# Performance work log

Measured on AMD Instinct MI355X. Metric: run time of the kernel, lower is better.

## Reference

```python
import jax, jax.numpy as jnp
import numpy as np

U = 1024  # utterance_size
H = 1024  # hidden_size
B = 32
T = 256


def _gru_cell(x, h, w_ih, w_hh, b_ih, b_hh):
    # torch.nn.GRUCell math
    gi = x @ w_ih.T + b_ih
    gh = h @ w_hh.T + b_hh
    i_r, i_z, i_n = jnp.split(gi, 3, axis=-1)
    h_r, h_z, h_n = jnp.split(gh, 3, axis=-1)
    r = jax.nn.sigmoid(i_r + h_r)
    z = jax.nn.sigmoid(i_z + h_z)
    n = jnp.tanh(i_n + r * h_n)
    return (1.0 - z) * n + z * h


def setup_inputs() -> dict:
    key = jax.random.key(0)
    ks = jax.random.split(key, 15)
    su = 1.0 / np.sqrt(U)
    sh = 1.0 / np.sqrt(H)

    def unif(k, shape, s):
        return jax.random.uniform(k, shape, jnp.float32, -s, s)

    inputs = jax.random.normal(ks[0], (B, T, U), jnp.float32)
    global_W = jax.random.normal(ks[1], (U, U), jnp.float32)
    gW_ih = unif(ks[2], (3 * U, U), su)
    gW_hh = unif(ks[3], (3 * U, U), su)
    gb_ih = unif(ks[4], (3 * U,), su)
    gb_hh = unif(ks[5], (3 * U,), su)
    pW_ih = unif(ks[6], (3 * U, U), su)
    pW_hh = unif(ks[7], (3 * U, U), su)
    pb_ih = unif(ks[8], (3 * U,), su)
    pb_hh = unif(ks[9], (3 * U,), su)
    eW_ih = unif(ks[10], (3 * H, U), sh)
    eW_hh = unif(ks[11], (3 * H, H), sh)
    eb_ih = unif(ks[12], (3 * H,), sh)
    eb_hh = unif(ks[13], (3 * H,), sh)
    return dict(inputs=inputs, global_W=global_W,
                gW_ih=gW_ih, gW_hh=gW_hh, gb_ih=gb_ih, gb_hh=gb_hh,
                pW_ih=pW_ih, pW_hh=pW_hh, pb_ih=pb_ih, pb_hh=pb_hh,
                eW_ih=eW_ih, eW_hh=eW_hh, eb_ih=eb_ih, eb_hh=eb_hh)


def _forward(inputs, global_W, gW_ih, gW_hh, gb_ih, gb_hh,
             pW_ih, pW_hh, pb_ih, pb_hh, eW_ih, eW_hh, eb_ih, eb_hh):
    Bb, Tt, Uu = inputs.shape
    Hh = eW_hh.shape[-1]
    x = jnp.transpose(inputs, (1, 0, 2))  # (T, B, U)
    hist0 = jnp.zeros((Tt + 1, Bb, Uu), inputs.dtype)  # global_s history, index 0 = zero init
    g0 = jnp.zeros((Bb, Uu), inputs.dtype)
    p0_0 = jnp.zeros((Bb, Uu), inputs.dtype)
    p1_0 = jnp.zeros((Bb, Uu), inputs.dtype)
    e0 = jnp.zeros((Bb, Hh), inputs.dtype)
    time_idx = jnp.arange(Tt + 1)

    def step(carry, xi):
        hist, g, p0, p1, e = carry
        ut, i = xi
        is_even = (i % 2) == 0
        p_cur = jnp.where(is_even, p0, p1)  # party_s[cur_party]
        g_new = _gru_cell(ut + p_cur, g, gW_ih, gW_hh, gb_ih, gb_hh)
        hist = hist.at[i + 1].set(g_new)  # appended but NOT attended this step
        # attention over global_s[0:i+1] (zero init + g_0..g_{i-1})
        q = ut @ global_W  # (B, U)
        scores = jnp.einsum('tbu,bu->tb', hist, q)  # (T+1, B)
        mask = time_idx[:, None] <= i
        scores = jnp.where(mask, scores, -jnp.inf)
        alpha = jax.nn.softmax(scores, axis=0)  # softmax over history dim
        ct = jnp.einsum('tb,tbu->bu', alpha, hist)
        p_new = _gru_cell(ut + ct, p_cur, pW_ih, pW_hh, pb_ih, pb_hh)
        p0 = jnp.where(is_even, p_new, p0)
        p1 = jnp.where(is_even, p1, p_new)
        e_new = _gru_cell(p_new, e, eW_ih, eW_hh, eb_ih, eb_hh)
        return (hist, g_new, p0, p1, e_new), e_new

    _, outs = jax.lax.scan(step, (hist0, g0, p0_0, p1_0, e0), (x, jnp.arange(Tt)))
    return jnp.transpose(outs, (1, 0, 2))  # (B, T, H)


def reference(inputs, global_W, gW_ih, gW_hh, gb_ih, gb_hh,
              pW_ih, pW_hh, pb_ih, pb_hh, eW_ih, eW_hh, eb_ih, eb_hh):
    return _forward(inputs, global_W, gW_ih, gW_hh, gb_ih, gb_hh,
                    pW_ih, pW_hh, pb_ih, pb_hh, eW_ih, eW_hh, eb_ih, eb_hh)
```

## Files before the change

### kernel.cpp

```cpp
#include <hip/hip_runtime.h>
#include <math.h>

#define UU 1024
#define BB 32
#define TT 256
#define NCHUNK 2
#define GRIDN 256
#define RING 32

#define WPS   6291456u
#define WCELL (2u * WPS)
#define SR  0u
#define SZ  2097152u
#define SNX 4194304u
#define SNH 5242880u
#define APS   65536u
#define ASLOT (2u * APS)
#define AEX(u, b) ((((((u) >> 5) * 4 + (((u) >> 3) & 3)) * 32 + (b)) * 8) + ((u) & 7))

#define SCR_OFF  131072
#define RED_OFF  147456
#define FLAG_OFF 147520
#define LDSB     147584

typedef __attribute__((ext_vector_type(8))) short bf16x8;
typedef __attribute__((ext_vector_type(4))) float f32x4;
#define MF(a, b, c) __builtin_amdgcn_mfma_f32_16x16x32_bf16((a), (b), (c), 0, 0, 0)

__device__ __forceinline__ ushort bf16rne(float v) {
    uint x = __float_as_uint(v);
    uint r = (x + 0x7fffu + ((x >> 16) & 1u)) >> 16;
    return (ushort)r;
}
__device__ __forceinline__ float ubf2f(ushort u) {
    return __uint_as_float(((uint)u) << 16);
}
__device__ __forceinline__ void split2(float v, ushort& h, ushort& l) {
    h = bf16rne(v);
    l = bf16rne(v - ubf2f(h));
}
__device__ __forceinline__ void store_f32_sc(float* p, float v) {
    asm volatile("global_store_dword %0, %1, off sc1" :: "v"(p), "v"(v) : "memory");
}
__device__ __forceinline__ void store_u16_sc(ushort* p, ushort v) {
    uint vv = v;
    asm volatile("global_store_short %0, %1, off sc1" :: "v"(p), "v"(vv) : "memory");
}
__device__ __forceinline__ void vm_drain() {
    asm volatile("s_waitcnt vmcnt(0)" ::: "memory");
}
__device__ __forceinline__ float load_f32_ag(const float* p) {
    return __hip_atomic_load(p, __ATOMIC_RELAXED, __HIP_MEMORY_SCOPE_AGENT);
}
__device__ __forceinline__ int load_i32_ag(const int* p) {
    return __hip_atomic_load(p, __ATOMIC_RELAXED, __HIP_MEMORY_SCOPE_AGENT);
}
__device__ __forceinline__ bf16x8 load_frag_ag(const ushort* p) {
    union { unsigned long long q[2]; bf16x8 v; } u;
    u.q[0] = __hip_atomic_load((const unsigned long long*)p,
                               __ATOMIC_RELAXED, __HIP_MEMORY_SCOPE_AGENT);
    u.q[1] = __hip_atomic_load((const unsigned long long*)(p + 4),
                               __ATOMIC_RELAXED, __HIP_MEMORY_SCOPE_AGENT);
    return u.v;
}

__global__ void packw_kernel(const float* __restrict__ gWih, const float* __restrict__ gWhh,
                             const float* __restrict__ pWih, const float* __restrict__ pWhh,
                             const float* __restrict__ eWih, const float* __restrict__ eWhh,
                             ushort* __restrict__ wpack) {
    int cellb = blockIdx.x / 12288;
    int tile = blockIdx.x - cellb * 12288;
    const float* Wih = (cellb == 0) ? gWih : (cellb == 1) ? pWih : eWih;
    const float* Whh = (cellb == 0) ? gWhh : (cellb == 1) ? pWhh : eWhh;
    ushort* wp = wpack + (size_t)cellb * WCELL;
    int sec, jt, ks, nks;
    size_t soff;
    if (tile < 8192) {
        sec = tile >> 12; int l = tile & 4095; jt = l >> 6; ks = l & 63; nks = 64;
        soff = sec ? SZ : SR;
    } else {
        int l2 = tile - 8192; sec = 2 + (l2 >> 11); int l = l2 & 2047; jt = l >> 5; ks = l & 31; nks = 32;
        soff = (sec == 2) ? SNX : SNH;
    }
    int p = threadIdx.x;
    int e0 = (p & 3) * 2, ul = (p >> 2) & 15, hi = p >> 6;
    int u = jt * 16 + ul;
    int kk = ks * 32 + hi * 8 + e0;
    float2 w;
    if (sec < 2) {
        int row = (sec ? 1024 : 0) + u;
        if (kk < 1024) w = *(const float2*)&Wih[(size_t)row * UU + kk];
        else           w = *(const float2*)&Whh[(size_t)row * UU + kk - 1024];
    } else if (sec == 2) {
        w = *(const float2*)&Wih[(size_t)(2048 + u) * UU + kk];
    } else {
        w = *(const float2*)&Whh[(size_t)(2048 + u) * UU + kk];
    }
    ushort h0, l0, h1, l1;
    split2(w.x, h0, l0); split2(w.y, h1, l1);
    size_t ob = soff + ((((size_t)jt * nks + ks) * 4 + hi) * 16 + ul) * 8 + e0;
    *(uint*)(wp + ob)       = (uint)h0 | ((uint)h1 << 16);
    *(uint*)(wp + WPS + ob) = (uint)l0 | ((uint)l1 << 16);
}

__global__ __launch_bounds__(256)
void qall_kernel(const float* __restrict__ x,
                 const float* __restrict__ gW,
                 float* __restrict__ q) {
    __shared__ float xs[16][257];
    __shared__ float gws[16][128];
    const int r0 = blockIdx.x * 256, n0 = blockIdx.y * 128;
    const int tid = threadIdx.x;
    const int tr = tid & 31, tn = tid >> 5;
    float acc[8][16];
    #pragma unroll
    for (int i = 0; i < 8; ++i)
        #pragma unroll
        for (int j = 0; j < 16; ++j) acc[i][j] = 0.f;
    for (int k0 = 0; k0 < UU; k0 += 16) {
        {
            int rr = tid >> 2;
            const int f4 = (tid & 3) * 4;
            #pragma unroll
            for (int it = 0; it < 4; ++it, rr += 64) {
                const int r = r0 + rr;
                const int tt = r >> 5, bb = r & 31;
                float4 v = *(const float4*)&x[((size_t)bb * TT + tt) * UU + k0 + f4];
                xs[f4][rr] = v.x; xs[f4 + 1][rr] = v.y;
                xs[f4 + 2][rr] = v.z; xs[f4 + 3][rr] = v.w;
            }
        }
        {
            int kr = tid >> 5;
            const int nn = (tid & 31) * 4;
            #pragma unroll
            for (int it = 0; it < 2; ++it, kr += 8) {
                float4 v = *(const float4*)&gW[(size_t)(k0 + kr) * UU + n0 + nn];
                *(float4*)&gws[kr][nn] = v;
            }
        }
        __syncthreads();
        #pragma unroll
        for (int kk = 0; kk < 16; ++kk) {
            float xv[8];
            #pragma unroll
            for (int i = 0; i < 8; ++i) xv[i] = xs[kk][tr + 32 * i];
            float gv[16];
            #pragma unroll
            for (int j4 = 0; j4 < 4; ++j4) {
                float4 g = *(const float4*)&gws[kk][tn * 16 + j4 * 4];
                gv[j4 * 4] = g.x; gv[j4 * 4 + 1] = g.y;
                gv[j4 * 4 + 2] = g.z; gv[j4 * 4 + 3] = g.w;
            }
            #pragma unroll
            for (int i = 0; i < 8; ++i)
                #pragma unroll
                for (int j = 0; j < 16; ++j)
                    acc[i][j] += xv[i] * gv[j];
        }
        __syncthreads();
    }
    #pragma unroll
    for (int i = 0; i < 8; ++i) {
        const int r = r0 + tr + 32 * i;
        #pragma unroll
        for (int j4 = 0; j4 < 4; ++j4) {
            float4 v = {acc[i][j4 * 4], acc[i][j4 * 4 + 1],
                        acc[i][j4 * 4 + 2], acc[i][j4 * 4 + 3]};
            *(float4*)&q[(size_t)r * UU + n0 + tn * 16 + j4 * 4] = v;
        }
    }
}

__global__ void init_kernel(const float* __restrict__ inputs,
                            const float* __restrict__ gbih, const float* __restrict__ gbhh,
                            const float* __restrict__ pbih, const float* __restrict__ pbhh,
                            const float* __restrict__ ebih, const float* __restrict__ ebhh,
                            float* __restrict__ hist, float* __restrict__ Pf,
                            ushort* __restrict__ gpack, ushort* __restrict__ ppack,
                            ushort* __restrict__ epack, float* __restrict__ biasp,
                            int* __restrict__ cnt, int* __restrict__ bar) {
    if (blockIdx.x == 0) {
        if (threadIdx.x < 32) cnt[threadIdx.x] = 0;
        for (int i = threadIdx.x; i < 1024; i += 256) bar[i] = 0;
    }
    if (blockIdx.x < 128) {
        int i = blockIdx.x * 256 + threadIdx.x;
        int b = i >> 10, u = i & 1023;
        hist[i] = 0.f;
        Pf[i] = 0.f; Pf[32768 + i] = 0.f;
        int ex = AEX(u, b);
        int eh = ex + 32768;
        gpack[eh] = 0; gpack[APS + eh] = 0;
        ppack[eh] = 0; ppack[APS + eh] = 0;
        ppack[ASLOT + eh] = 0; ppack[ASLOT + APS + eh] = 0;
        epack[eh] = 0; epack[APS + eh] = 0;
        float x0 = inputs[((size_t)b * TT + 0) * UU + u];
        float x1 = inputs[((size_t)b * TT + 1) * UU + u];
        ushort h, l;
        split2(x0, h, l); gpack[ex] = h; gpack[APS + ex] = l;
        split2(x1, h, l); gpack[ASLOT + ex] = h; gpack[ASLOT + APS + ex] = l;
    } else {
        int idx = (blockIdx.x - 128) * 256 + threadIdx.x;
        int cell = idx >> 12, g4 = (idx >> 10) & 3, u = idx & 1023;
        const float* bih = (cell == 0) ? gbih : (cell == 1) ? pbih : ebih;
        const float* bhh = (cell == 0) ? gbhh : (cell == 1) ? pbhh : ebhh;
        float v;
        if (g4 == 0) v = bih[u] + bhh[u];
        else if (g4 == 1) v = bih[1024 + u] + bhh[1024 + u];
        else if (g4 == 2) v = bih[2048 + u];
        else v = bhh[2048 + u];
        biasp[idx] = v;
    }
}

__global__ __launch_bounds__(512)
__attribute__((amdgpu_waves_per_eu(2)))
void persist_kernel(const float* __restrict__ inputs,
                    const ushort* __restrict__ wpack,
                    const float* __restrict__ biasp,
                    ushort* __restrict__ gpack, ushort* __restrict__ ppack,
                    ushort* __restrict__ epack,
                    float* __restrict__ hist, float* __restrict__ Pf,
                    const float* __restrict__ qall,
                    float* __restrict__ out,
                    float* __restrict__ attC, float* __restrict__ attML,
                    int* __restrict__ cnt, int* __restrict__ bar) {
    extern __shared__ char smraw[];
    float* lds_scr  = (float*)(smraw + SCR_OFF);
    float* lds_red  = (float*)(smraw + RED_OFF);
    int*   lds_flag = (int*)(smraw + FLAG_OFF);

    const int blk = blockIdx.x, tid = threadIdx.x;
    const int cell = blk >> 6, jt = blk & 63;
    const int w = tid >> 6, lane = tid & 63;
    const int l15 = lane & 15, hi4 = lane >> 4;
    const int ab = blk & 31, ac = (blk >> 5) & 1;
    const ushort* wp = wpack + (size_t)cell * WCELL;

    if (cell < 3) {
        bf16x8 whiR[8], whiZ[8], whiN[8], wloN[8];
        const int ebt = tid >> 8, eli = (tid >> 2) & 63, ei = tid & 3;
        const int eb = ebt * 16 + (eli & 15);
        const int eu = jt * 16 + (eli >> 4) * 4 + ei;
        const int eex = AEX(eu, eb);
        #pragma unroll
        for (int i = 0; i < 8; ++i) {
            const int ks = w * 8 + i;
            const size_t aoff = ((size_t)(jt * 256 + ks * 4 + hi4)) * 128 + (size_t)l15 * 8;
            whiR[i] = *(const bf16x8*)(wp + SR + aoff);
            whiZ[i] = *(const bf16x8*)(wp + SZ + aoff);
            bf16x8 rlo = *(const bf16x8*)(wp + SR + WPS + aoff);
            bf16x8 zlo = *(const bf16x8*)(wp + SZ + WPS + aoff);
            *(bf16x8*)(smraw + (((w * 16 + i) * 64 + lane) << 4)) = rlo;
            *(bf16x8*)(smraw + (((w * 16 + 8 + i) * 64 + lane) << 4)) = zlo;
            const int ksn = (w & 3) * 8 + i;
            const size_t noff = ((size_t)(jt * 128 + ksn * 4 + hi4)) * 128 + (size_t)l15 * 8;
            const size_t sN = (w < 4) ? SNX : SNH;
            whiN[i] = *(const bf16x8*)(wp + sN + noff);
            wloN[i] = *(const bf16x8*)(wp + sN + WPS + noff);
        }
        const float* bc = biasp + cell * 4096;
        const float bR = bc[eu], bZ = bc[1024 + eu];
        const float bNI = bc[2048 + eu], bNH = bc[3072 + eu];
        ushort* apk = (cell == 0) ? gpack : (cell == 1) ? ppack : epack;
        __syncthreads();

        for (int tc = 0; tc < TT; ++tc) {
            if (w == 0) {
                const int* wptr; int wneed;
                if (cell == 0) {
                    if (lane == 0)      { wptr = bar;       wneed = tc; }
                    else if (lane == 1) { wptr = bar + 32;  wneed = tc - 1; }
                    else                { wptr = bar;       wneed = -2147483647; }
                } else if (cell == 1) {
                    if (lane < 32)       { wptr = bar + 512 + lane * 16; wneed = tc + 1; }
                    else if (lane == 32) { wptr = bar + 32; wneed = tc - 1; }
                    else if (lane == 33) { wptr = bar + 64; wneed = tc - 31; }
                    else                 { wptr = bar;      wneed = -2147483647; }
                } else {
                    if (lane == 0)      { wptr = bar + 32;  wneed = tc + 1; }
                    else if (lane == 1) { wptr = bar + 64;  wneed = tc; }
                    else                { wptr = bar;       wneed = -2147483647; }
                }
                while (!__all(load_i32_ag(wptr) >= wneed))
                    __builtin_amdgcn_s_sleep(8);
            }
            __syncthreads();
            f32x4 aR0 = {0,0,0,0}, aR1 = {0,0,0,0};
            f32x4 aZ0 = {0,0,0,0}, aZ1 = {0,0,0,0};
            f32x4 aN0 = {0,0,0,0}, aN1 = {0,0,0,0};
            const ushort* ap = apk + (size_t)(tc & (RING - 1)) * ASLOT;
            const ushort* bbp = ap + ((size_t)hi4 * 32 + l15) * 8;
            #pragma unroll
            for (int i = 0; i < 8; ++i) {
                const int ks = w * 8 + i;
                const ushort* bp = bbp + (size_t)ks * 1024;
                bf16x8 bh0 = load_frag_ag(bp);
                bf16x8 bh1 = load_frag_ag(bp + 128);
                bf16x8 bl0 = load_frag_ag(bp + APS);
                bf16x8 bl1 = load_frag_ag(bp + APS + 128);
                bf16x8 rlo = *(const bf16x8*)(smraw + (((w * 16 + i) * 64 + lane) << 4));
                bf16x8 zlo = *(const bf16x8*)(smraw + (((w * 16 + 8 + i) * 64 + lane) << 4));
                aR0 = MF(whiR[i], bh0, aR0); aR0 = MF(whiR[i], bl0, aR0); aR0 = MF(rlo, bh0, aR0);
                aR1 = MF(whiR[i], bh1, aR1); aR1 = MF(whiR[i], bl1, aR1); aR1 = MF(rlo, bh1, aR1);
                aZ0 = MF(whiZ[i], bh0, aZ0); aZ0 = MF(whiZ[i], bl0, aZ0); aZ0 = MF(zlo, bh0, aZ0);
                aZ1 = MF(whiZ[i], bh1, aZ1); aZ1 = MF(whiZ[i], bl1, aZ1); aZ1 = MF(zlo, bh1, aZ1);
                aN0 = MF(whiN[i], bh0, aN0); aN0 = MF(whiN[i], bl0, aN0); aN0 = MF(wloN[i], bh0, aN0);
                aN1 = MF(whiN[i], bh1, aN1); aN1 = MF(whiN[i], bl1, aN1); aN1 = MF(wloN[i], bh1, aN1);
            }
            float R, Z, iN, hN;
            *(f32x4*)&lds_scr[((0 * 8 + w) * 64 + lane) * 4] = aR0;
            *(f32x4*)&lds_scr[((1 * 8 + w) * 64 + lane) * 4] = aR1;
            __syncthreads();
            {
                float s = 0.f;
                #pragma unroll
                for (int w2 = 0; w2 < 8; ++w2) s += lds_scr[((ebt * 8 + w2) * 64 + eli) * 4 + ei];
                R = s;
            }
            __syncthreads();
            *(f32x4*)&lds_scr[((0 * 8 + w) * 64 + lane) * 4] = aZ0;
            *(f32x4*)&lds_scr[((1 * 8 + w) * 64 + lane) * 4] = aZ1;
            __syncthreads();
            {
                float s = 0.f;
                #pragma unroll
                for (int w2 = 0; w2 < 8; ++w2) s += lds_scr[((ebt * 8 + w2) * 64 + eli) * 4 + ei];
                Z = s;
            }
            __syncthreads();
            *(f32x4*)&lds_scr[((0 * 8 + w) * 64 + lane) * 4] = aN0;
            *(f32x4*)&lds_scr[((1 * 8 + w) * 64 + lane) * 4] = aN1;
            __syncthreads();
            {
                float si = 0.f, sh = 0.f;
                #pragma unroll
                for (int w2 = 0; w2 < 4; ++w2) si += lds_scr[((ebt * 8 + w2) * 64 + eli) * 4 + ei];
                #pragma unroll
                for (int w2 = 4; w2 < 8; ++w2) sh += lds_scr[((ebt * 8 + w2) * 64 + eli) * 4 + ei];
                iN = si; hN = sh;
            }
            {
                float hprev;
                if (cell == 0)      hprev = hist[((size_t)tc * BB + eb) * UU + eu];
                else if (cell == 1) hprev = load_f32_ag(&Pf[(size_t)(tc & (RING - 1)) * BB * UU + (size_t)eb * UU + eu]);
                else                hprev = (tc > 0) ? out[((size_t)eb * TT + tc - 1) * UU + eu] : 0.f;
                const float r = 1.f / (1.f + expf(-(R + bR)));
                const float z = 1.f / (1.f + expf(-(Z + bZ)));
                const float n2 = tanhf(iN + bNI + r * (hN + bNH));
                const float val = (1.f - z) * n2 + z * hprev;
                ushort vh, vl; split2(val, vh, vl);
                if (cell == 0) {
                    store_f32_sc(&hist[((size_t)(tc + 1) * BB + eb) * UU + eu], val);
                    ushort* d = gpack + (size_t)((tc + 1) & (RING - 1)) * ASLOT;
                    store_u16_sc(d + eex + 32768, vh);
                    store_u16_sc(d + APS + eex + 32768, vl);
                } else if (cell == 1) {
                    ushort* d = epack + (size_t)(tc & (RING - 1)) * ASLOT;
                    store_u16_sc(d + eex, vh);
                    store_u16_sc(d + APS + eex, vl);
                    if (tc + 2 < TT) {
                        store_f32_sc(&Pf[(size_t)((tc + 2) & (RING - 1)) * BB * UU + (size_t)eb * UU + eu], val);
                        ushort* d2 = ppack + (size_t)((tc + 2) & (RING - 1)) * ASLOT;
                        store_u16_sc(d2 + eex + 32768, vh);
                        store_u16_sc(d2 + APS + eex + 32768, vl);
                        const float gx = val + inputs[((size_t)eb * TT + tc + 2) * UU + eu];
                        ushort gh, gl; split2(gx, gh, gl);
                        ushort* d3 = gpack + (size_t)((tc + 2) & (RING - 1)) * ASLOT;
                        store_u16_sc(d3 + eex, gh);
                        store_u16_sc(d3 + APS + eex, gl);
                    }
                } else {
                    store_f32_sc(&out[((size_t)eb * TT + tc) * UU + eu], val);
                    if (tc + 1 < TT) {
                        ushort* d = epack + (size_t)((tc + 1) & (RING - 1)) * ASLOT;
                        store_u16_sc(d + eex + 32768, vh);
                        store_u16_sc(d + APS + eex + 32768, vl);
                    }
                }
            }
            vm_drain();
            __syncthreads();
            if (tid == 0) {
                int* ring = bar + 128 + cell * 128 + (tc & 3) * 32;
                int old = __hip_atomic_fetch_add(ring, 1, __ATOMIC_RELAXED,
                                                 __HIP_MEMORY_SCOPE_AGENT);
                if ((old & 63) == 63) {
                    (void)__hip_atomic_fetch_max(bar + cell * 32, tc + 1,
                                                 __ATOMIC_RELAXED, __HIP_MEMORY_SCOPE_AGENT);
                }
            }
        }
    } else {
        int* fin = bar + 512 + ab * 16;
        for (int t = 0; t < TT; ++t) {
            if (w == 0) {
                const int* wptr; int wneed;
                if (lane == 0)      { wptr = bar; wneed = t; }
                else if (lane == 1) { wptr = fin; wneed = t; }
                else                { wptr = bar; wneed = -2147483647; }
                while (!__all(load_i32_ag(wptr) >= wneed))
                    __builtin_amdgcn_s_sleep(8);
            }
            __syncthreads();
            const int slot = t & 3;
            float* aC = attC + (((size_t)slot * NCHUNK + ac) * BB + ab) * UU;
            float* aML = attML + (((size_t)slot * NCHUNK + ac) * BB + ab) * 2;
            const int nt2 = t + 1;
            const int cstr = (nt2 + NCHUNK - 1) / NCHUNK;
            const int r0 = ac * cstr;
            const int r1x = r0 + cstr;
            const int r1 = (r1x < nt2) ? r1x : nt2;
            const int n = r1 - r0;
            if (n <= 0) {
                #pragma unroll
                for (int rep = 0; rep < 2; ++rep)
                    store_f32_sc(aC + tid + rep * 512, 0.f);
                if (tid == 0) {
                    store_f32_sc(aML, -INFINITY);
                    store_f32_sc(aML + 1, 0.f);
                }
            } else {
                const float* qb = qall + ((size_t)t * BB + ab) * UU;
                float4 q0 = *(const float4*)&qb[lane * 4];
                float4 q1 = *(const float4*)&qb[256 + lane * 4];
                float4 q2 = *(const float4*)&qb[512 + lane * 4];
                float4 q3 = *(const float4*)&qb[768 + lane * 4];
                float m_run = -INFINITY, l_run = 0.f;
                float4 c0 = {0,0,0,0}, c1 = {0,0,0,0}, c2 = {0,0,0,0}, c3 = {0,0,0,0};
                for (int tp = r0 + w; tp < r1; tp += 8) {
                    const float* hr = hist + ((size_t)tp * BB + ab) * UU;
                    float4 h0 = *(const float4*)&hr[lane * 4];
                    float4 h1 = *(const float4*)&hr[256 + lane * 4];
                    float4 h2 = *(const float4*)&hr[512 + lane * 4];
                    float4 h3 = *(const float4*)&hr[768 + lane * 4];
                    float s = h0.x*q0.x + h0.y*q0.y + h0.z*q0.z + h0.w*q0.w
                            + h1.x*q1.x + h1.y*q1.y + h1.z*q1.z + h1.w*q1.w
                            + h2.x*q2.x + h2.y*q2.y + h2.z*q2.z + h2.w*q2.w
                            + h3.x*q3.x + h3.y*q3.y + h3.z*q3.z + h3.w*q3.w;
                    #pragma unroll
                    for (int off = 32; off; off >>= 1) s += __shfl_xor(s, off);
                    const float mn = fmaxf(m_run, s);
                    const float sc = expf(m_run - mn);
                    const float e2 = expf(s - mn);
                    c0.x = c0.x*sc + e2*h0.x; c0.y = c0.y*sc + e2*h0.y; c0.z = c0.z*sc + e2*h0.z; c0.w = c0.w*sc + e2*h0.w;
                    c1.x = c1.x*sc + e2*h1.x; c1.y = c1.y*sc + e2*h1.y; c1.z = c1.z*sc + e2*h1.z; c1.w = c1.w*sc + e2*h1.w;
                    c2.x = c2.x*sc + e2*h2.x; c2.y = c2.y*sc + e2*h2.y; c2.z = c2.z*sc + e2*h2.z; c2.w = c2.w*sc + e2*h2.w;
                    c3.x = c3.x*sc + e2*h3.x; c3.y = c3.y*sc + e2*h3.y; c3.z = c3.z*sc + e2*h3.z; c3.w = c3.w*sc + e2*h3.w;
                    l_run = l_run * sc + e2;
                    m_run = mn;
                }
                *(float4*)&lds_scr[w * 512 + lane * 4] = c0;
                *(float4*)&lds_scr[w * 512 + 256 + lane * 4] = c1;
                if (lane == 0) { lds_red[w] = m_run; lds_red[8 + w] = l_run; }
                __syncthreads();
                float M = lds_red[0];
                #pragma unroll
                for (int k = 1; k < 8; ++k) M = fmaxf(M, lds_red[k]);
                float ww[8], L = 0.f;
                #pragma unroll
                for (int k = 0; k < 8; ++k) { ww[k] = expf(lds_red[k] - M); L += ww[k] * lds_red[8 + k]; }
                if (tid == 0) {
                    store_f32_sc(aML, M);
                    store_f32_sc(aML + 1, L);
                }
                {
                    float s = 0.f;
                    #pragma unroll
                    for (int w2 = 0; w2 < 8; ++w2) s += ww[w2] * lds_scr[w2 * 512 + tid];
                    store_f32_sc(aC + tid, s);
                }
                __syncthreads();
                *(float4*)&lds_scr[w * 512 + lane * 4] = c2;
                *(float4*)&lds_scr[w * 512 + 256 + lane * 4] = c3;
                __syncthreads();
                {
                    float s = 0.f;
                    #pragma unroll
                    for (int w2 = 0; w2 < 8; ++w2) s += ww[w2] * lds_scr[w2 * 512 + tid];
                    store_f32_sc(aC + 512 + tid, s);
                }
            }
            vm_drain();
            __syncthreads();
            if (tid == 0) {
                int old = __hip_atomic_fetch_add(cnt + ab, 1, __ATOMIC_RELAXED,
                                                 __HIP_MEMORY_SCOPE_AGENT);
                lds_flag[0] = (old & 1);
            }
            __syncthreads();
            if (lds_flag[0]) {
                float mm[NCHUNK], ll[NCHUNK];
                #pragma unroll
                for (int c = 0; c < NCHUNK; ++c) {
                    const float* ml = attML + (((size_t)slot * NCHUNK + c) * BB + ab) * 2;
                    mm[c] = load_f32_ag(ml);
                    ll[c] = load_f32_ag(ml + 1);
                }
                float M2 = mm[0];
                #pragma unroll
                for (int c = 1; c < NCHUNK; ++c) M2 = fmaxf(M2, mm[c]);
                float den = 0.f, wc[NCHUNK];
                #pragma unroll
                for (int c = 0; c < NCHUNK; ++c) { wc[c] = expf(mm[c] - M2); den += wc[c] * ll[c]; }
                const float inv = 1.f / den;
                ushort* d = ppack + (size_t)(t & (RING - 1)) * ASLOT;
                #pragma unroll
                for (int rep = 0; rep < 2; ++rep) {
                    const int e = tid + rep * 512;
                    float s3 = 0.f;
                    #pragma unroll
                    for (int c = 0; c < NCHUNK; ++c)
                        s3 += wc[c] * load_f32_ag(&attC[(((size_t)slot * NCHUNK + c) * BB + ab) * UU + e]);
                    const float xv = s3 * inv + inputs[((size_t)ab * TT + t) * UU + e];
                    ushort vh2, vl2; split2(xv, vh2, vl2);
                    const int ex2 = AEX(e, ab);
                    store_u16_sc(d + ex2, vh2);
                    store_u16_sc(d + APS + ex2, vl2);
                }
                vm_drain();
            }
            __syncthreads();
            if (tid == 0 && lds_flag[0])
                __hip_atomic_fetch_add(fin, 1, __ATOMIC_RELAXED, __HIP_MEMORY_SCOPE_AGENT);
        }
    }
}

extern "C" void kernel_launch(void* const* d_in, const int* in_sizes, int n_in,
                              void* d_out, int out_size, void* d_ws, size_t ws_size,
                              hipStream_t stream) {
    (void)in_sizes; (void)n_in; (void)out_size; (void)ws_size;
    const float* inputs = (const float*)d_in[0];
    const float* gW   = (const float*)d_in[1];
    const float* gWih = (const float*)d_in[2];
    const float* gWhh = (const float*)d_in[3];
    const float* gbih = (const float*)d_in[4];
    const float* gbhh = (const float*)d_in[5];
    const float* pWih = (const float*)d_in[6];
    const float* pWhh = (const float*)d_in[7];
    const float* pbih = (const float*)d_in[8];
    const float* pbhh = (const float*)d_in[9];
    const float* eWih = (const float*)d_in[10];
    const float* eWhh = (const float*)d_in[11];
    const float* ebih = (const float*)d_in[12];
    const float* ebhh = (const float*)d_in[13];
    float* out = (float*)d_out;

    char* ws = (char*)d_ws;
    size_t off = 0;
    auto alloc = [&](size_t bytes) {
        void* p = ws + off;
        off += (bytes + 255) & ~(size_t)255;
        return p;
    };
    ushort* wpack = (ushort*)alloc((size_t)3 * WCELL * 2);
    ushort* gpack = (ushort*)alloc((size_t)RING * ASLOT * 2);
    ushort* ppack = (ushort*)alloc((size_t)RING * ASLOT * 2);
    ushort* epack = (ushort*)alloc((size_t)RING * ASLOT * 2);
    float* hist  = (float*)alloc((size_t)(TT + 1) * BB * UU * 4);
    float* qall  = (float*)alloc((size_t)TT * BB * UU * 4);
    float* Pf    = (float*)alloc((size_t)RING * BB * UU * 4);
    float* biasp = (float*)alloc((size_t)3 * 4096 * 4);
    float* attC  = (float*)alloc((size_t)4 * NCHUNK * BB * UU * 4);
    float* attML = (float*)alloc((size_t)4 * NCHUNK * BB * 2 * 4);
    int*   cnt   = (int*)alloc(32 * 4);
    int*   bar   = (int*)alloc(1024 * 4);

    packw_kernel<<<36864, 256, 0, stream>>>(gWih, gWhh, pWih, pWhh, eWih, eWhh, wpack);
    qall_kernel<<<dim3(32, 8), 256, 0, stream>>>(inputs, gW, qall);
    init_kernel<<<176, 256, 0, stream>>>(inputs, gbih, gbhh, pbih, pbhh, ebih, ebhh,
                                         hist, Pf, gpack, ppack, epack, biasp, cnt, bar);

    hipFuncSetAttribute((const void*)persist_kernel,
                        hipFuncAttributeMaxDynamicSharedMemorySize, LDSB);
    void* args[] = {(void*)&inputs, (void*)&wpack, (void*)&biasp,
                    (void*)&gpack, (void*)&ppack, (void*)&epack,
                    (void*)&hist, (void*)&Pf, (void*)&qall, (void*)&out,
                    (void*)&attC, (void*)&attML, (void*)&cnt, (void*)&bar};
    hipError_t ce = hipLaunchCooperativeKernel((const void*)persist_kernel,
                                               dim3(GRIDN), dim3(512), args,
                                               (unsigned)LDSB, stream);
    if (ce != hipSuccess) {
        (void)hipGetLastError();
        persist_kernel<<<GRIDN, 512, LDSB, stream>>>(inputs, wpack, biasp,
                                                     gpack, ppack, epack,
                                                     hist, Pf, qall, out,
                                                     attC, attML, cnt, bar);
    }
}
```

Before: 2.828 ms.

## Keep Z low weights in registers and merge gate reductions into one barrier

The low bf16 part of the Z-gate weights now stays in registers instead of LDS, which halves the LDS weight stash and lets the scratch region shrink and move. The three serial LDS cross-wave reductions (R, Z, N), each guarded by two barriers, become a single write phase, one barrier, and one read phase. The spin-wait sleep interval is also shortened so waiting blocks react to flag updates sooner. Costs are higher register pressure, a larger scratch footprint, and more polling traffic on the flags.

```diff
diff --git a/kernel.cpp b/kernel.cpp
--- a/kernel.cpp
+++ b/kernel.cpp
@@ -18,10 +18,10 @@
 #define ASLOT (2u * APS)
 #define AEX(u, b) ((((((u) >> 5) * 4 + (((u) >> 3) & 3)) * 32 + (b)) * 8) + ((u) & 7))
 
-#define SCR_OFF  131072
-#define RED_OFF  147456
-#define FLAG_OFF 147520
-#define LDSB     147584
+#define SCR_OFF  65536
+#define RED_OFF  114688
+#define FLAG_OFF 114752
+#define LDSB     114816
 
 typedef __attribute__((ext_vector_type(8))) short bf16x8;
 typedef __attribute__((ext_vector_type(4))) float f32x4;
@@ -239,7 +239,7 @@
     const ushort* wp = wpack + (size_t)cell * WCELL;
 
     if (cell < 3) {
-        bf16x8 whiR[8], whiZ[8], whiN[8], wloN[8];
+        bf16x8 whiR[8], whiZ[8], wloZ[8], whiN[8], wloN[8];
         const int ebt = tid >> 8, eli = (tid >> 2) & 63, ei = tid & 3;
         const int eb = ebt * 16 + (eli & 15);
         const int eu = jt * 16 + (eli >> 4) * 4 + ei;
@@ -251,9 +251,8 @@
             whiR[i] = *(const bf16x8*)(wp + SR + aoff);
             whiZ[i] = *(const bf16x8*)(wp + SZ + aoff);
             bf16x8 rlo = *(const bf16x8*)(wp + SR + WPS + aoff);
-            bf16x8 zlo = *(const bf16x8*)(wp + SZ + WPS + aoff);
-            *(bf16x8*)(smraw + (((w * 16 + i) * 64 + lane) << 4)) = rlo;
-            *(bf16x8*)(smraw + (((w * 16 + 8 + i) * 64 + lane) << 4)) = zlo;
+            wloZ[i] = *(const bf16x8*)(wp + SZ + WPS + aoff);
+            *(bf16x8*)(smraw + (((w * 8 + i) * 64 + lane) << 4)) = rlo;
             const int ksn = (w & 3) * 8 + i;
             const size_t noff = ((size_t)(jt * 128 + ksn * 4 + hi4)) * 128 + (size_t)l15 * 8;
             const size_t sN = (w < 4) ? SNX : SNH;
@@ -284,7 +283,7 @@
                     else                { wptr = bar;       wneed = -2147483647; }
                 }
                 while (!__all(load_i32_ag(wptr) >= wneed))
-                    __builtin_amdgcn_s_sleep(8);
+                    __builtin_amdgcn_s_sleep(2);
             }
             __syncthreads();
             f32x4 aR0 = {0,0,0,0}, aR1 = {0,0,0,0};
@@ -300,47 +299,34 @@
                 bf16x8 bh1 = load_frag_ag(bp + 128);
                 bf16x8 bl0 = load_frag_ag(bp + APS);
                 bf16x8 bl1 = load_frag_ag(bp + APS + 128);
-                bf16x8 rlo = *(const bf16x8*)(smraw + (((w * 16 + i) * 64 + lane) << 4));
-                bf16x8 zlo = *(const bf16x8*)(smraw + (((w * 16 + 8 + i) * 64 + lane) << 4));
+                bf16x8 rlo = *(const bf16x8*)(smraw + (((w * 8 + i) * 64 + lane) << 4));
                 aR0 = MF(whiR[i], bh0, aR0); aR0 = MF(whiR[i], bl0, aR0); aR0 = MF(rlo, bh0, aR0);
                 aR1 = MF(whiR[i], bh1, aR1); aR1 = MF(whiR[i], bl1, aR1); aR1 = MF(rlo, bh1, aR1);
-                aZ0 = MF(whiZ[i], bh0, aZ0); aZ0 = MF(whiZ[i], bl0, aZ0); aZ0 = MF(zlo, bh0, aZ0);
-                aZ1 = MF(whiZ[i], bh1, aZ1); aZ1 = MF(whiZ[i], bl1, aZ1); aZ1 = MF(zlo, bh1, aZ1);
+                aZ0 = MF(whiZ[i], bh0, aZ0); aZ0 = MF(whiZ[i], bl0, aZ0); aZ0 = MF(wloZ[i], bh0, aZ0);
+                aZ1 = MF(whiZ[i], bh1, aZ1); aZ1 = MF(whiZ[i], bl1, aZ1); aZ1 = MF(wloZ[i], bh1, aZ1);
                 aN0 = MF(whiN[i], bh0, aN0); aN0 = MF(whiN[i], bl0, aN0); aN0 = MF(wloN[i], bh0, aN0);
                 aN1 = MF(whiN[i], bh1, aN1); aN1 = MF(whiN[i], bl1, aN1); aN1 = MF(wloN[i], bh1, aN1);
             }
-            float R, Z, iN, hN;
-            *(f32x4*)&lds_scr[((0 * 8 + w) * 64 + lane) * 4] = aR0;
-            *(f32x4*)&lds_scr[((1 * 8 + w) * 64 + lane) * 4] = aR1;
-            __syncthreads();
-            {
-                float s = 0.f;
-                #pragma unroll
-                for (int w2 = 0; w2 < 8; ++w2) s += lds_scr[((ebt * 8 + w2) * 64 + eli) * 4 + ei];
-                R = s;
-            }
-            __syncthreads();
-            *(f32x4*)&lds_scr[((0 * 8 + w) * 64 + lane) * 4] = aZ0;
-            *(f32x4*)&lds_scr[((1 * 8 + w) * 64 + lane) * 4] = aZ1;
-            __syncthreads();
-            {
-                float s = 0.f;
-                #pragma unroll
-                for (int w2 = 0; w2 < 8; ++w2) s += lds_scr[((ebt * 8 + w2) * 64 + eli) * 4 + ei];
-                Z = s;
-            }
-            __syncthreads();
-            *(f32x4*)&lds_scr[((0 * 8 + w) * 64 + lane) * 4] = aN0;
-            *(f32x4*)&lds_scr[((1 * 8 + w) * 64 + lane) * 4] = aN1;
-            __syncthreads();
-            {
-                float si = 0.f, sh = 0.f;
-                #pragma unroll
-                for (int w2 = 0; w2 < 4; ++w2) si += lds_scr[((ebt * 8 + w2) * 64 + eli) * 4 + ei];
-                #pragma unroll
-                for (int w2 = 4; w2 < 8; ++w2) sh += lds_scr[((ebt * 8 + w2) * 64 + eli) * 4 + ei];
-                iN = si; hN = sh;
-            }
+            *(f32x4*)&lds_scr[(((0 * 2 + 0) * 8 + w) * 64 + lane) * 4] = aR0;
+            *(f32x4*)&lds_scr[(((0 * 2 + 1) * 8 + w) * 64 + lane) * 4] = aR1;
+            *(f32x4*)&lds_scr[(((1 * 2 + 0) * 8 + w) * 64 + lane) * 4] = aZ0;
+            *(f32x4*)&lds_scr[(((1 * 2 + 1) * 8 + w) * 64 + lane) * 4] = aZ1;
+            *(f32x4*)&lds_scr[(((2 * 2 + 0) * 8 + w) * 64 + lane) * 4] = aN0;
+            *(f32x4*)&lds_scr[(((2 * 2 + 1) * 8 + w) * 64 + lane) * 4] = aN1;
+            __syncthreads();
+            float R = 0.f, Z = 0.f, iN = 0.f, hN = 0.f;
+            #pragma unroll
+            for (int w2 = 0; w2 < 8; ++w2)
+                R += lds_scr[(((0 * 2 + ebt) * 8 + w2) * 64 + eli) * 4 + ei];
+            #pragma unroll
+            for (int w2 = 0; w2 < 8; ++w2)
+                Z += lds_scr[(((1 * 2 + ebt) * 8 + w2) * 64 + eli) * 4 + ei];
+            #pragma unroll
+            for (int w2 = 0; w2 < 4; ++w2)
+                iN += lds_scr[(((2 * 2 + ebt) * 8 + w2) * 64 + eli) * 4 + ei];
+            #pragma unroll
+            for (int w2 = 4; w2 < 8; ++w2)
+                hN += lds_scr[(((2 * 2 + ebt) * 8 + w2) * 64 + eli) * 4 + ei];
             {
                 float hprev;
                 if (cell == 0)      hprev = hist[((size_t)tc * BB + eb) * UU + eu];
@@ -401,7 +387,7 @@
                 else if (lane == 1) { wptr = fin; wneed = t; }
                 else                { wptr = bar; wneed = -2147483647; }
                 while (!__all(load_i32_ag(wptr) >= wneed))
-                    __builtin_amdgcn_s_sleep(8);
+                    __builtin_amdgcn_s_sleep(2);
             }
             __syncthreads();
             const int slot = t & 3;
```

Result: slower. 2.891 ms (+2.2%).
